# Kernel tuning notes

Hardware: AMD Instinct MI355X
Metric: run time of the kernel (lower is better)

## Reference

```python
import jax, jax.numpy as jnp
import numpy as np

CELL = 128
STEPS = 20
N_KEYS = 4   # ['first_conn','second_conn','first_op','second_op']
N_OUT = 6


def setup_inputs() -> dict:
    key = jax.random.key(0)
    ks = jax.random.split(key, 10)
    s = 0.05
    return {
        "net": jax.random.randint(ks[0], (STEPS,), 0, N_OUT),          # sampled actions, each in [0,6)
        "reward": jax.random.uniform(ks[1], (1,), dtype=jnp.float32),   # unused in forward (kept for signature parity)
        "emb_start": jax.random.normal(ks[2], (1, CELL), jnp.float32) * s,          # Embedding(1,128)
        "emb_keys": jax.random.normal(ks[3], (N_KEYS, N_OUT, CELL), jnp.float32) * s,
        "fc_W": jax.random.normal(ks[4], (N_KEYS, N_OUT, CELL), jnp.float32) * s,
        "fc_b": jax.random.normal(ks[5], (N_KEYS, N_OUT), jnp.float32) * s,
        "W_ih": jax.random.normal(ks[6], (4 * CELL, CELL), jnp.float32) * s,  # LSTMCell input weights (i,f,g,o)
        "W_hh": jax.random.normal(ks[7], (4 * CELL, CELL), jnp.float32) * s,  # LSTMCell hidden weights
        "b_ih": jax.random.normal(ks[8], (4 * CELL,), jnp.float32) * s,
        "b_hh": jax.random.normal(ks[9], (4 * CELL,), jnp.float32) * s,
    }


def _lstm_cell(x, h, c, W_ih, W_hh, b_ih, b_hh):
    # PyTorch LSTMCell: gates ordered (i, f, g, o)
    gates = x @ W_ih.T + b_ih + h @ W_hh.T + b_hh   # [1, 4*CELL]
    i, f, g, o = jnp.split(gates, 4, axis=-1)
    c_new = jax.nn.sigmoid(f) * c + jax.nn.sigmoid(i) * jnp.tanh(g)
    h_new = jax.nn.sigmoid(o) * jnp.tanh(c_new)
    return h_new, c_new


def reference(net, reward, emb_start, emb_keys, fc_W, fc_b, W_ih, W_hh, b_ih, b_hh):
    key_idx = jnp.arange(STEPS) % N_KEYS            # which head/embedding at each step
    fc_W_t = fc_W[key_idx]                          # [STEPS, 6, CELL]
    fc_b_t = fc_b[key_idx]                          # [STEPS, 6]
    emb_t = emb_keys[key_idx, net]                  # [STEPS, CELL] next-step input embedding

    def step(carry, xs):
        h, c, x = carry
        Wt, bt, ev = xs
        h, c = _lstm_cell(x, h, c, W_ih, W_hh, b_ih, b_hh)
        probs = jax.nn.softmax(h @ Wt.T + bt, axis=1)   # [1, 6]
        return (h, c, ev[None, :]), probs

    h0 = jnp.zeros((1, CELL), dtype=emb_start.dtype)
    c0 = jnp.zeros((1, CELL), dtype=emb_start.dtype)
    x0 = emb_start                                   # embedding lookup of action 0 in a 1-row table
    _, outputs = jax.lax.scan(step, (h0, c0, x0), (fc_W_t, fc_b_t, emb_t))
    return outputs                                   # [STEPS, 1, 6], stacked version of the torch list
```

## Files before the change

### kernel.cpp

```cpp
#include <hip/hip_runtime.h>
#include <hip/hip_fp16.h>

#define CELL 128
#define STEPS 20

typedef _Float16 half8_t __attribute__((ext_vector_type(8)));
typedef float    floatx4 __attribute__((ext_vector_type(4)));

__device__ __forceinline__ unsigned packf2(float x, float y) {
    typedef _Float16 h2 __attribute__((ext_vector_type(2)));
    h2 h = { (_Float16)x, (_Float16)y };
    return __builtin_bit_cast(unsigned, h);
}
__device__ __forceinline__ float fdot2u(unsigned a, unsigned b, float c) {
    typedef _Float16 h2 __attribute__((ext_vector_type(2)));
#if __has_builtin(__builtin_amdgcn_fdot2)
    return __builtin_amdgcn_fdot2(__builtin_bit_cast(h2, a), __builtin_bit_cast(h2, b), c, false);
#else
    h2 x = __builtin_bit_cast(h2, a), y = __builtin_bit_cast(h2, b);
    return fmaf((float)x[0], (float)y[0], fmaf((float)x[1], (float)y[1], c));
#endif
}
__device__ __forceinline__ float fastrcp(float x) {
#if __has_builtin(__builtin_amdgcn_rcpf)
    return __builtin_amdgcn_rcpf(x);
#else
    return 1.0f / x;
#endif
}
__device__ __forceinline__ float sig_rcp(float x) {
    return fastrcp(1.0f + __expf(-x));
}
__device__ __forceinline__ float tanh_rcp(float x) {
    return fmaf(2.0f, fastrcp(1.0f + __expf(-2.0f * x)), -1.0f);
}
__device__ __forceinline__ half8_t cvt8(const float* p) {
    const float4* p4 = (const float4*)p;
    float4 a = p4[0], b = p4[1];
    return half8_t{ (_Float16)a.x, (_Float16)a.y, (_Float16)a.z, (_Float16)a.w,
                    (_Float16)b.x, (_Float16)b.y, (_Float16)b.z, (_Float16)b.w };
}

extern "C" __global__ void __launch_bounds__(512, 1)
nas_policy_kernel(const int* __restrict__ net,
                  const float* __restrict__ emb_start,
                  const float* __restrict__ emb_keys,
                  const float* __restrict__ fc_W,
                  const float* __restrict__ fc_b,
                  const float* __restrict__ W_ih,
                  const float* __restrict__ W_hh,
                  const float* __restrict__ b_ih,
                  const float* __restrict__ b_hh,
                  float* __restrict__ out)
{
    const int t0   = threadIdx.x;
    const int wv   = t0 >> 6;
    const int lane = t0 & 63;
    const int quad = lane >> 4;
    const int lcol = lane & 15;

    __shared__ __align__(16) unsigned  s_xv2[32 * 68];
    __shared__ __align__(16) float     s_gx[STEPS * 512];
    __shared__ __align__(16) _Float16  hbuf[2 * 128];
    __shared__ unsigned s_fcw2[24 * 64];
    __shared__ float    s_fcb[24];
    __shared__ float    llog[STEPS * 8];

    for (int i = t0; i < STEPS * 64; i += 512) {
        const int m = i >> 6, j = i & 63;
        const float2* src = (m == 0) ? (const float2*)emb_start
            : (const float2*)(emb_keys + ((((m - 1) & 3) * 6) + net[m - 1]) * CELL);
        float2 v = src[j];
        s_xv2[m * 68 + j] = packf2(v.x, v.y);
    }
    {
        const float2* fw2 = (const float2*)fc_W;
        for (int i = t0; i < 24 * 64; i += 512) { float2 w = fw2[i]; s_fcw2[i] = packf2(w.x, w.y); }
    }
    if (t0 < 24)  s_fcb[t0] = fc_b[t0];
    if (t0 < 128) hbuf[128 + t0] = (_Float16)0.0f;

    const int rr0 = (wv << 4) + lcol;
    float biasx[4];
#pragma unroll
    for (int tau = 0; tau < 4; ++tau) {
        const int r = tau * 128 + rr0;
        biasx[tau] = b_ih[r] + b_hh[r];
    }

    __syncthreads();

    {
        half8_t bw[4][4];
#pragma unroll
        for (int kc = 0; kc < 4; ++kc) {
            const int k0 = kc * 32 + quad * 8;
#pragma unroll
            for (int tau = 0; tau < 4; ++tau)
                bw[kc][tau] = cvt8(W_ih + (tau * 128 + rr0) * CELL + k0);
        }
        floatx4 ax0[4] = { {0,0,0,0}, {0,0,0,0}, {0,0,0,0}, {0,0,0,0} };
        floatx4 ax1[4] = { {0,0,0,0}, {0,0,0,0}, {0,0,0,0}, {0,0,0,0} };
#pragma unroll
        for (int kc = 0; kc < 4; ++kc) {
            uint4 u0 = *(const uint4*)&s_xv2[lcol * 68 + kc * 16 + quad * 4];
            uint4 u1 = *(const uint4*)&s_xv2[(16 + lcol) * 68 + kc * 16 + quad * 4];
            half8_t a0f = __builtin_bit_cast(half8_t, u0);
            half8_t a1f = __builtin_bit_cast(half8_t, u1);
#pragma unroll
            for (int tau = 0; tau < 4; ++tau) {
                ax0[tau] = __builtin_amdgcn_mfma_f32_16x16x32_f16(a0f, bw[kc][tau], ax0[tau], 0, 0, 0);
                ax1[tau] = __builtin_amdgcn_mfma_f32_16x16x32_f16(a1f, bw[kc][tau], ax1[tau], 0, 0, 0);
            }
        }
#pragma unroll
        for (int tau = 0; tau < 4; ++tau) {
#pragma unroll
            for (int reg = 0; reg < 4; ++reg)
                s_gx[(quad * 4 + reg) * 512 + rr0 * 4 + tau] = ax0[tau][reg] + biasx[tau];
            if (quad == 0) {
#pragma unroll
                for (int reg = 0; reg < 4; ++reg)
                    s_gx[(16 + reg) * 512 + rr0 * 4 + tau] = ax1[tau][reg] + biasx[tau];
            }
        }
    }

    half8_t bf0[4], bf1[4], bf2[4], bf3[4];
#pragma unroll
    for (int kc = 0; kc < 4; ++kc) {
        const int k0 = kc * 32 + quad * 8;
        bf0[kc] = cvt8(W_hh + (0 * 128 + rr0) * CELL + k0);
        bf1[kc] = cvt8(W_hh + (1 * 128 + rr0) * CELL + k0);
        bf2[kc] = cvt8(W_hh + (2 * 128 + rr0) * CELL + k0);
        bf3[kc] = cvt8(W_hh + (3 * 128 + rr0) * CELL + k0);
    }

    float c = 0.0f;
    __syncthreads();

    for (int t = 0; t < STEPS; ++t) {
        const uint4* hp4 = (const uint4*)(hbuf + (((t + 1) & 1) << 7));
        floatx4 gx = *(const floatx4*)&s_gx[t * 512 + rr0 * 4];
        floatx4 a0a = {0,0,0,0}, a0b = {0,0,0,0}, a1a = {0,0,0,0}, a1b = {0,0,0,0};
        floatx4 a2a = {0,0,0,0}, a2b = {0,0,0,0}, a3a = {0,0,0,0}, a3b = {0,0,0,0};
        {
            uint4 u0 = hp4[(0 << 2) + quad], u1 = hp4[(1 << 2) + quad];
            uint4 u2 = hp4[(2 << 2) + quad], u3 = hp4[(3 << 2) + quad];
            half8_t f0 = __builtin_bit_cast(half8_t, u0), f1 = __builtin_bit_cast(half8_t, u1);
            half8_t f2 = __builtin_bit_cast(half8_t, u2), f3 = __builtin_bit_cast(half8_t, u3);
            a0a = __builtin_amdgcn_mfma_f32_16x16x32_f16(f0, bf0[0], a0a, 0, 0, 0);
            a1a = __builtin_amdgcn_mfma_f32_16x16x32_f16(f0, bf1[0], a1a, 0, 0, 0);
            a2a = __builtin_amdgcn_mfma_f32_16x16x32_f16(f0, bf2[0], a2a, 0, 0, 0);
            a3a = __builtin_amdgcn_mfma_f32_16x16x32_f16(f0, bf3[0], a3a, 0, 0, 0);
            a0b = __builtin_amdgcn_mfma_f32_16x16x32_f16(f1, bf0[1], a0b, 0, 0, 0);
            a1b = __builtin_amdgcn_mfma_f32_16x16x32_f16(f1, bf1[1], a1b, 0, 0, 0);
            a2b = __builtin_amdgcn_mfma_f32_16x16x32_f16(f1, bf2[1], a2b, 0, 0, 0);
            a3b = __builtin_amdgcn_mfma_f32_16x16x32_f16(f1, bf3[1], a3b, 0, 0, 0);
            a0a = __builtin_amdgcn_mfma_f32_16x16x32_f16(f2, bf0[2], a0a, 0, 0, 0);
            a1a = __builtin_amdgcn_mfma_f32_16x16x32_f16(f2, bf1[2], a1a, 0, 0, 0);
            a2a = __builtin_amdgcn_mfma_f32_16x16x32_f16(f2, bf2[2], a2a, 0, 0, 0);
            a3a = __builtin_amdgcn_mfma_f32_16x16x32_f16(f2, bf3[2], a3a, 0, 0, 0);
            a0b = __builtin_amdgcn_mfma_f32_16x16x32_f16(f3, bf0[3], a0b, 0, 0, 0);
            a1b = __builtin_amdgcn_mfma_f32_16x16x32_f16(f3, bf1[3], a1b, 0, 0, 0);
            a2b = __builtin_amdgcn_mfma_f32_16x16x32_f16(f3, bf2[3], a2b, 0, 0, 0);
            a3b = __builtin_amdgcn_mfma_f32_16x16x32_f16(f3, bf3[3], a3b, 0, 0, 0);
        }

        if (t >= 1 && wv < 6 && quad == 1) {
            const int li = lcol;
            const int hg = ((t - 1) & 3) * 6 + wv;
            const unsigned* hb = (const unsigned*)(hbuf + (((t + 1) & 1) << 7));
            const unsigned* wp = s_fcw2 + hg * 64 + li * 4;
            float p = fdot2u(hb[li * 4],     wp[0], 0.0f);
            p = fdot2u(hb[li * 4 + 1], wp[1], p);
            p = fdot2u(hb[li * 4 + 2], wp[2], p);
            p = fdot2u(hb[li * 4 + 3], wp[3], p);
            p += __shfl_down(p, 8); p += __shfl_down(p, 4);
            p += __shfl_down(p, 2); p += __shfl_down(p, 1);
            if (li == 0) llog[(t - 1) * 8 + wv] = p + s_fcb[hg];
        }

        {
            float ig = sig_rcp (a0a[0] + a0b[0] + gx[0]);
            float fg = sig_rcp (a1a[0] + a1b[0] + gx[1]);
            float gg = tanh_rcp(a2a[0] + a2b[0] + gx[2]);
            float og = sig_rcp (a3a[0] + a3b[0] + gx[3]);
            c = fg * c + ig * gg;
            float h = og * tanh_rcp(c);
            if (quad == 0)
                hbuf[((t & 1) << 7) + rr0] = (_Float16)h;
        }

        __syncthreads();
    }

    if (wv < 6 && quad == 1) {
        const int li = lcol;
        const int hg = (19 & 3) * 6 + wv;
        const unsigned* hb = (const unsigned*)(hbuf + 128);
        const unsigned* wp = s_fcw2 + hg * 64 + li * 4;
        float p = fdot2u(hb[li * 4],     wp[0], 0.0f);
        p = fdot2u(hb[li * 4 + 1], wp[1], p);
        p = fdot2u(hb[li * 4 + 2], wp[2], p);
        p = fdot2u(hb[li * 4 + 3], wp[3], p);
        p += __shfl_down(p, 8); p += __shfl_down(p, 4);
        p += __shfl_down(p, 2); p += __shfl_down(p, 1);
        if (li == 0) llog[19 * 8 + wv] = p + s_fcb[hg];
    }
    __syncthreads();
    if (t0 < STEPS * 6) {
        const int s = t0 / 6, k = t0 - s * 6;
        const float* L = llog + s * 8;
        float l0 = L[0], l1 = L[1], l2 = L[2], l3 = L[3], l4 = L[4], l5 = L[5];
        float m = fmaxf(fmaxf(fmaxf(l0, l1), fmaxf(l2, l3)), fmaxf(l4, l5));
        float e0 = __expf(l0 - m), e1 = __expf(l1 - m), e2 = __expf(l2 - m);
        float e3 = __expf(l3 - m), e4 = __expf(l4 - m), e5 = __expf(l5 - m);
        float sum = ((e0 + e1) + (e2 + e3)) + (e4 + e5);
        float mine = (k == 0) ? e0 : (k == 1) ? e1 : (k == 2) ? e2
                   : (k == 3) ? e3 : (k == 4) ? e4 : e5;
        out[t0] = mine / sum;
    }
}

extern "C" void kernel_launch(void* const* d_in, const int* in_sizes, int n_in,
                              void* d_out, int out_size, void* d_ws, size_t ws_size,
                              hipStream_t stream) {
    (void)in_sizes; (void)n_in; (void)out_size; (void)d_ws; (void)ws_size;
    const int*   net       = (const int*)d_in[0];
    const float* emb_start = (const float*)d_in[2];
    const float* emb_keys  = (const float*)d_in[3];
    const float* fc_W      = (const float*)d_in[4];
    const float* fc_b      = (const float*)d_in[5];
    const float* W_ih      = (const float*)d_in[6];
    const float* W_hh      = (const float*)d_in[7];
    const float* b_ih      = (const float*)d_in[8];
    const float* b_hh      = (const float*)d_in[9];
    float*       out       = (float*)d_out;

    hipLaunchKernelGGL(nas_policy_kernel, dim3(1), dim3(512), 0, stream,
                       net, emb_start, emb_keys, fc_W, fc_b,
                       W_ih, W_hh, b_ih, b_hh, out);
}
```

Measured before the change: 98.34 us.

## Split LSTM into multi-block prep kernel and lean single-block recurrence

New measurement: 97.32 us. No clear change (-1.0%).

```diff
diff --git a/kernel.cpp b/kernel.cpp
--- a/kernel.cpp
+++ b/kernel.cpp
@@ -6,6 +6,12 @@
 
 typedef _Float16 half8_t __attribute__((ext_vector_type(8)));
 typedef float    floatx4 __attribute__((ext_vector_type(4)));
+
+#define WS_GX    0
+#define WS_WHH   40960
+#define WS_FCW   (40960 + 131072)
+#define WS_FCB   (WS_FCW + 6144)
+#define WS_NEED  (WS_FCB + 96)
 
 __device__ __forceinline__ unsigned packf2(float x, float y) {
     typedef _Float16 h2 __attribute__((ext_vector_type(2)));
@@ -28,12 +34,8 @@
     return 1.0f / x;
 #endif
 }
-__device__ __forceinline__ float sig_rcp(float x) {
-    return fastrcp(1.0f + __expf(-x));
-}
-__device__ __forceinline__ float tanh_rcp(float x) {
-    return fmaf(2.0f, fastrcp(1.0f + __expf(-2.0f * x)), -1.0f);
-}
+__device__ __forceinline__ float sig_rcp(float x)  { return fastrcp(1.0f + __expf(-x)); }
+__device__ __forceinline__ float tanh_rcp(float x) { return fmaf(2.0f, fastrcp(1.0f + __expf(-2.0f * x)), -1.0f); }
 __device__ __forceinline__ half8_t cvt8(const float* p) {
     const float4* p4 = (const float4*)p;
     float4 a = p4[0], b = p4[1];
@@ -41,17 +43,196 @@
                     (_Float16)b.x, (_Float16)b.y, (_Float16)b.z, (_Float16)b.w };
 }
 
+extern "C" __global__ void __launch_bounds__(256)
+nas_prep_kernel(const int* __restrict__ net,
+                const float* __restrict__ emb_start,
+                const float* __restrict__ emb_keys,
+                const float* __restrict__ fc_W,
+                const float* __restrict__ fc_b,
+                const float* __restrict__ W_ih,
+                const float* __restrict__ W_hh,
+                const float* __restrict__ b_ih,
+                const float* __restrict__ b_hh,
+                unsigned char* __restrict__ ws)
+{
+    const int b = blockIdx.x, tid = threadIdx.x;
+
+    if (b < 128) {
+        __shared__ float sx[STEPS][CELL];
+        for (int i = tid; i < STEPS * CELL; i += 256) {
+            const int t = i >> 7, k = i & 127;
+            sx[t][k] = (t == 0) ? emb_start[k]
+                     : emb_keys[((((t - 1) & 3) * 6) + net[t - 1]) * CELL + k];
+        }
+        __syncthreads();
+        const int row  = b * 4 + (tid >> 6);
+        const int lane = tid & 63;
+        const float2 w = ((const float2*)W_ih)[row * 64 + lane];
+        const float bias = b_ih[row] + b_hh[row];
+        const int tau = row >> 7, cell = row & 127;
+        float* gx = (float*)(ws + WS_GX);
+#pragma unroll
+        for (int t = 0; t < STEPS; ++t) {
+            const float2 xv = *(const float2*)&sx[t][lane * 2];
+            float p = fmaf(w.x, xv.x, w.y * xv.y);
+            p += __shfl_down(p, 32); p += __shfl_down(p, 16);
+            p += __shfl_down(p, 8);  p += __shfl_down(p, 4);
+            p += __shfl_down(p, 2);  p += __shfl_down(p, 1);
+            if (lane == 0) gx[t * 512 + cell * 4 + tau] = p + bias;
+        }
+    } else if (b < 160) {
+        const int F   = (b - 128) * 256 + tid;
+        const int g   = F >> 9;
+        const int m   = F & 511;
+        const int tau = g >> 2, kc = g & 3;
+        const int rr0 = ((m >> 6) << 4) + (m & 15);
+        const int qd  = (m >> 4) & 3;
+        const int k0  = kc * 32 + qd * 8;
+        half8_t h8 = cvt8(W_hh + (tau * 128 + rr0) * CELL + k0);
+        ((uint4*)(ws + WS_WHH))[g * 512 + m] = __builtin_bit_cast(uint4, h8);
+    } else {
+        const float2* fw2 = (const float2*)fc_W;
+        unsigned* fcw = (unsigned*)(ws + WS_FCW);
+        for (int i = tid; i < 24 * 64; i += 256) {
+            const float2 w = fw2[i];
+            fcw[i] = packf2(w.x, w.y);
+        }
+        if (tid < 24) ((float*)(ws + WS_FCB))[tid] = fc_b[tid];
+    }
+}
+
 extern "C" __global__ void __launch_bounds__(512, 1)
-nas_policy_kernel(const int* __restrict__ net,
-                  const float* __restrict__ emb_start,
-                  const float* __restrict__ emb_keys,
-                  const float* __restrict__ fc_W,
-                  const float* __restrict__ fc_b,
-                  const float* __restrict__ W_ih,
-                  const float* __restrict__ W_hh,
-                  const float* __restrict__ b_ih,
-                  const float* __restrict__ b_hh,
+nas_policy_kernel(const unsigned char* __restrict__ ws,
                   float* __restrict__ out)
+{
+    const int t0   = threadIdx.x;
+    const int wv   = t0 >> 6;
+    const int lane = t0 & 63;
+    const int quad = lane >> 4;
+    const int lcol = lane & 15;
+    const int rr0  = (wv << 4) + lcol;
+
+    __shared__ __align__(16) _Float16 hbuf[2 * 128];
+    __shared__ float llog[STEPS * 8];
+
+    const float*    ws_gx  = (const float*)(ws + WS_GX);
+    const uint4*    ws_whh = (const uint4*)(ws + WS_WHH);
+    const unsigned* ws_fcw = (const unsigned*)(ws + WS_FCW);
+    const float*    ws_fcb = (const float*)(ws + WS_FCB);
+
+    half8_t bf0[4], bf1[4], bf2[4], bf3[4];
+#pragma unroll
+    for (int kc = 0; kc < 4; ++kc) {
+        bf0[kc] = __builtin_bit_cast(half8_t, ws_whh[(0 * 4 + kc) * 512 + t0]);
+        bf1[kc] = __builtin_bit_cast(half8_t, ws_whh[(1 * 4 + kc) * 512 + t0]);
+        bf2[kc] = __builtin_bit_cast(half8_t, ws_whh[(2 * 4 + kc) * 512 + t0]);
+        bf3[kc] = __builtin_bit_cast(half8_t, ws_whh[(3 * 4 + kc) * 512 + t0]);
+    }
+    if (t0 < 128) hbuf[128 + t0] = (_Float16)0.0f;
+    floatx4 gx_cur = *(const floatx4*)&ws_gx[rr0 * 4];
+    float c = 0.0f;
+    __syncthreads();
+
+    for (int t = 0; t < STEPS; ++t) {
+        const uint4* hp4 = (const uint4*)(hbuf + (((t + 1) & 1) << 7));
+        const floatx4 gx = gx_cur;
+        if (t + 1 < STEPS)
+            gx_cur = *(const floatx4*)&ws_gx[(t + 1) * 512 + rr0 * 4];
+
+        floatx4 a0a = { gx[0], 0, 0, 0 }, a0b = { 0, 0, 0, 0 };
+        floatx4 a1a = { gx[1], 0, 0, 0 }, a1b = { 0, 0, 0, 0 };
+        floatx4 a2a = { gx[2], 0, 0, 0 }, a2b = { 0, 0, 0, 0 };
+        floatx4 a3a = { gx[3], 0, 0, 0 }, a3b = { 0, 0, 0, 0 };
+        {
+            uint4 u0 = hp4[(0 << 2) + quad], u1 = hp4[(1 << 2) + quad];
+            uint4 u2 = hp4[(2 << 2) + quad], u3 = hp4[(3 << 2) + quad];
+            half8_t f0 = __builtin_bit_cast(half8_t, u0), f1 = __builtin_bit_cast(half8_t, u1);
+            half8_t f2 = __builtin_bit_cast(half8_t, u2), f3 = __builtin_bit_cast(half8_t, u3);
+            a0a = __builtin_amdgcn_mfma_f32_16x16x32_f16(f0, bf0[0], a0a, 0, 0, 0);
+            a1a = __builtin_amdgcn_mfma_f32_16x16x32_f16(f0, bf1[0], a1a, 0, 0, 0);
+            a2a = __builtin_amdgcn_mfma_f32_16x16x32_f16(f0, bf2[0], a2a, 0, 0, 0);
+            a3a = __builtin_amdgcn_mfma_f32_16x16x32_f16(f0, bf3[0], a3a, 0, 0, 0);
+            a0b = __builtin_amdgcn_mfma_f32_16x16x32_f16(f1, bf0[1], a0b, 0, 0, 0);
+            a1b = __builtin_amdgcn_mfma_f32_16x16x32_f16(f1, bf1[1], a1b, 0, 0, 0);
+            a2b = __builtin_amdgcn_mfma_f32_16x16x32_f16(f1, bf2[1], a2b, 0, 0, 0);
+            a3b = __builtin_amdgcn_mfma_f32_16x16x32_f16(f1, bf3[1], a3b, 0, 0, 0);
+            a0a = __builtin_amdgcn_mfma_f32_16x16x32_f16(f2, bf0[2], a0a, 0, 0, 0);
+            a1a = __builtin_amdgcn_mfma_f32_16x16x32_f16(f2, bf1[2], a1a, 0, 0, 0);
+            a2a = __builtin_amdgcn_mfma_f32_16x16x32_f16(f2, bf2[2], a2a, 0, 0, 0);
+            a3a = __builtin_amdgcn_mfma_f32_16x16x32_f16(f2, bf3[2], a3a, 0, 0, 0);
+            a0b = __builtin_amdgcn_mfma_f32_16x16x32_f16(f3, bf0[3], a0b, 0, 0, 0);
+            a1b = __builtin_amdgcn_mfma_f32_16x16x32_f16(f3, bf1[3], a1b, 0, 0, 0);
+            a2b = __builtin_amdgcn_mfma_f32_16x16x32_f16(f3, bf2[3], a2b, 0, 0, 0);
+            a3b = __builtin_amdgcn_mfma_f32_16x16x32_f16(f3, bf3[3], a3b, 0, 0, 0);
+        }
+
+        if (t >= 1 && wv < 6 && quad == 1) {
+            const int li = lcol;
+            const int hg = ((t - 1) & 3) * 6 + wv;
+            const unsigned* hb = (const unsigned*)(hbuf + (((t + 1) & 1) << 7));
+            const uint4 wpv = *(const uint4*)(ws_fcw + hg * 64 + li * 4);
+            float p = fdot2u(hb[li * 4],     wpv.x, 0.0f);
+            p = fdot2u(hb[li * 4 + 1], wpv.y, p);
+            p = fdot2u(hb[li * 4 + 2], wpv.z, p);
+            p = fdot2u(hb[li * 4 + 3], wpv.w, p);
+            p += __shfl_down(p, 8); p += __shfl_down(p, 4);
+            p += __shfl_down(p, 2); p += __shfl_down(p, 1);
+            if (li == 0) llog[(t - 1) * 8 + wv] = p + ws_fcb[hg];
+        }
+
+        {
+            float ig = sig_rcp (a0a[0] + a0b[0]);
+            float fg = sig_rcp (a1a[0] + a1b[0]);
+            float gg = tanh_rcp(a2a[0] + a2b[0]);
+            float og = sig_rcp (a3a[0] + a3b[0]);
+            c = fg * c + ig * gg;
+            float h = og * tanh_rcp(c);
+            if (quad == 0)
+                hbuf[((t & 1) << 7) + rr0] = (_Float16)h;
+        }
+
+        __syncthreads();
+    }
+
+    if (wv < 6 && quad == 1) {
+        const int li = lcol;
+        const int hg = (19 & 3) * 6 + wv;
+        const unsigned* hb = (const unsigned*)(hbuf + 128);
+        const uint4 wpv = *(const uint4*)(ws_fcw + hg * 64 + li * 4);
+        float p = fdot2u(hb[li * 4],     wpv.x, 0.0f);
+        p = fdot2u(hb[li * 4 + 1], wpv.y, p);
+        p = fdot2u(hb[li * 4 + 2], wpv.z, p);
+        p = fdot2u(hb[li * 4 + 3], wpv.w, p);
+        p += __shfl_down(p, 8); p += __shfl_down(p, 4);
+        p += __shfl_down(p, 2); p += __shfl_down(p, 1);
+        if (li == 0) llog[19 * 8 + wv] = p + ws_fcb[hg];
+    }
+    __syncthreads();
+    if (t0 < STEPS * 6) {
+        const int s = t0 / 6, k = t0 - s * 6;
+        const float* L = llog + s * 8;
+        float l0 = L[0], l1 = L[1], l2 = L[2], l3 = L[3], l4 = L[4], l5 = L[5];
+        float m = fmaxf(fmaxf(fmaxf(l0, l1), fmaxf(l2, l3)), fmaxf(l4, l5));
+        float e0 = __expf(l0 - m), e1 = __expf(l1 - m), e2 = __expf(l2 - m);
+        float e3 = __expf(l3 - m), e4 = __expf(l4 - m), e5 = __expf(l5 - m);
+        float sum = ((e0 + e1) + (e2 + e3)) + (e4 + e5);
+        float mine = (k == 0) ? e0 : (k == 1) ? e1 : (k == 2) ? e2
+                   : (k == 3) ? e3 : (k == 4) ? e4 : e5;
+        out[t0] = mine / sum;
+    }
+}
+
+extern "C" __global__ void __launch_bounds__(512, 1)
+nas_policy_mono(const int* __restrict__ net,
+                const float* __restrict__ emb_start,
+                const float* __restrict__ emb_keys,
+                const float* __restrict__ fc_W,
+                const float* __restrict__ fc_b,
+                const float* __restrict__ W_ih,
+                const float* __restrict__ W_hh,
+                const float* __restrict__ b_ih,
+                const float* __restrict__ b_hh,
+                float* __restrict__ out)
 {
     const int t0   = threadIdx.x;
     const int wv   = t0 >> 6;
@@ -226,7 +407,7 @@
 extern "C" void kernel_launch(void* const* d_in, const int* in_sizes, int n_in,
                               void* d_out, int out_size, void* d_ws, size_t ws_size,
                               hipStream_t stream) {
-    (void)in_sizes; (void)n_in; (void)out_size; (void)d_ws; (void)ws_size;
+    (void)in_sizes; (void)n_in; (void)out_size;
     const int*   net       = (const int*)d_in[0];
     const float* emb_start = (const float*)d_in[2];
     const float* emb_keys  = (const float*)d_in[3];
@@ -238,7 +419,16 @@
     const float* b_hh      = (const float*)d_in[9];
     float*       out       = (float*)d_out;
 
-    hipLaunchKernelGGL(nas_policy_kernel, dim3(1), dim3(512), 0, stream,
-                       net, emb_start, emb_keys, fc_W, fc_b,
-                       W_ih, W_hh, b_ih, b_hh, out);
-}
+    if (d_ws != nullptr && ws_size >= (size_t)WS_NEED) {
+        unsigned char* ws = (unsigned char*)d_ws;
+        hipLaunchKernelGGL(nas_prep_kernel, dim3(161), dim3(256), 0, stream,
+                           net, emb_start, emb_keys, fc_W, fc_b,
+                           W_ih, W_hh, b_ih, b_hh, ws);
+        hipLaunchKernelGGL(nas_policy_kernel, dim3(1), dim3(512), 0, stream,
+                           (const unsigned char*)ws, out);
+    } else {
+        hipLaunchKernelGGL(nas_policy_mono, dim3(1), dim3(512), 0, stream,
+                           net, emb_start, emb_keys, fc_W, fc_b,
+                           W_ih, W_hh, b_ih, b_hh, out);
+    }
+}
```
